# Performance work log

Hardware: AMD Instinct MI355X
Metric: run time of the kernel (lower is better)

## Reference

```python
import jax, jax.numpy as jnp
import numpy as np

B, D_IN, H, N_LAYERS, D_OUT = 262144, 8, 128, 3, 1


def setup_inputs() -> dict:
    key = jax.random.key(0)
    ks = jax.random.split(key, 18)
    rn = lambda k, shape, fan: (jax.random.normal(k, shape, jnp.float32) / np.sqrt(fan))
    return {
        "x": jax.random.normal(ks[0], (B, D_IN), jnp.float32),
        "Sw_w": rn(ks[1], (D_IN, H), D_IN),
        "Sw_b": rn(ks[2], (H,), D_IN),
        "Uz": rn(ks[3], (N_LAYERS, D_IN, H), D_IN),
        "Wsz_w": rn(ks[4], (N_LAYERS, H, H), H),
        "Wsz_b": rn(ks[5], (N_LAYERS, H), H),
        "Ug": rn(ks[6], (N_LAYERS, D_IN, H), D_IN),
        "Wsg_w": rn(ks[7], (N_LAYERS, H, H), H),
        "Wsg_b": rn(ks[8], (N_LAYERS, H), H),
        "Ur": rn(ks[9], (N_LAYERS, D_IN, H), D_IN),
        "Wsr_w": rn(ks[10], (N_LAYERS, H, H), H),
        "Wsr_b": rn(ks[11], (N_LAYERS, H), H),
        "Uh": rn(ks[12], (N_LAYERS, D_IN, H), D_IN),
        "Wsh_w": rn(ks[13], (N_LAYERS, H, H), H),
        "Wsh_b": rn(ks[14], (N_LAYERS, H), H),
        "Wf_w": rn(ks[15], (H, D_OUT), H),
        "Wf_b": rn(ks[16], (D_OUT,), H),
    }


def reference(x, Sw_w, Sw_b, Uz, Wsz_w, Wsz_b, Ug, Wsg_w, Wsg_b,
              Ur, Wsr_w, Wsr_b, Uh, Wsh_w, Wsh_b, Wf_w, Wf_b):
    # x: [B, D_in]; S: [B, H]
    S = x @ Sw_w + Sw_b
    n = Uz.shape[0]
    for i in range(n):  # small fixed layer count
        S = jax.nn.sigmoid(S)
        Z = jax.nn.sigmoid(x @ Uz[i] + S @ Wsz_w[i] + Wsz_b[i])
        G = jax.nn.sigmoid(x @ Ug[i] + S @ Wsg_w[i] + Wsg_b[i])
        R = jax.nn.sigmoid(x @ Ur[i] + S @ Wsr_w[i] + Wsr_b[i])
        H_ = jnp.tanh(x @ Uh[i] + (S * R) @ Wsh_w[i] + Wsh_b[i])
        S = (1.0 - G) * H_ + Z * S
    return S @ Wf_w + Wf_b  # [B, D_out]
```

## Files before the change

### kernel.cpp

```cpp
#include <hip/hip_runtime.h>

typedef __bf16 bf16_t;
typedef __bf16 bf16x4 __attribute__((ext_vector_type(4)));
typedef __bf16 bf16x8 __attribute__((ext_vector_type(8)));
typedef float f32x4 __attribute__((ext_vector_type(4)));

#define NL 3
#define HD 128
#define ROWS 64
#define SSTR 152
#define RSTR 136
#define THREADS 512
#define BATCH 262144
#define NBLK (BATCH / ROWS)

#define SW_OFF 0
#define U_OFF  4096
#define W_OFF  53248
#define WS_ELEMS 249856

#define MFMA(a, b, c) __builtin_amdgcn_mfma_f32_16x16x32_bf16((a), (b), (c), 0, 0, 0)

#define LOG2E 1.4426950408889634f
__device__ __forceinline__ float sige(float a) {
    return __builtin_amdgcn_rcpf(1.f + __builtin_amdgcn_exp2f(a));
}
__device__ __forceinline__ float tanhe(float a) {
    return 1.f - 2.f * __builtin_amdgcn_rcpf(__builtin_amdgcn_exp2f(a) + 1.f);
}
__device__ __forceinline__ float sigm(float v) {
    return __builtin_amdgcn_rcpf(1.f + __builtin_amdgcn_exp2f(-LOG2E * v));
}

__global__ void dgm_prep(const float* __restrict__ SwW, const float* __restrict__ Swb,
                         const float* __restrict__ Uz, const float* __restrict__ Wz, const float* __restrict__ Bz,
                         const float* __restrict__ Ug, const float* __restrict__ Wg, const float* __restrict__ Bg,
                         const float* __restrict__ Ur, const float* __restrict__ Wr, const float* __restrict__ Br,
                         const float* __restrict__ Uh, const float* __restrict__ Wh,
                         bf16_t* __restrict__ ws) {
    int idx = blockIdx.x * 256 + threadIdx.x;
    if (idx >= WS_ELEMS) return;
    const float* Us[4] = {Uz, Ug, Ur, Uh};
    const float* Wm[4] = {Wz, Wg, Wr, Wh};
    const float gsc[4] = {-LOG2E, LOG2E, -LOG2E, 2.f * LOG2E};
    if (idx < U_OFF) {
        int ct = idx >> 9, rem = idx & 511, lane = rem >> 3, j = rem & 7;
        int q = lane >> 4, mm = lane & 15;
        int k = q * 8 + j, n = ct * 16 + mm;
        float v = (k < 8) ? SwW[k * HD + n] : (k == 8) ? Swb[n] : 0.f;
        ws[idx] = (bf16_t)(v * -LOG2E);
    } else if (idx < W_OFF) {
        int t = idx - U_OFF;
        int lg = t >> 12, r2 = t & 4095;
        int l = lg >> 2, g = lg & 3;
        int ct = r2 >> 9, rem = r2 & 511, lane = rem >> 3, j = rem & 7;
        int q = lane >> 4, mm = lane & 15;
        int k = q * 8 + j, n = ct * 16 + mm;
        const float* Bs = (g == 0) ? Bz : (g == 1) ? Bg : (g == 2) ? Br : (const float*)0;
        float v = (k < 8) ? Us[g][(l * 8 + k) * HD + n]
                : (k == 8 && g < 3) ? Bs[l * HD + n] : 0.f;
        ws[idx] = (bf16_t)(v * gsc[g]);
    } else {
        int t = idx - W_OFF;
        int lg = t >> 14, r2 = t & 16383;
        int l = lg >> 2, g = lg & 3;
        int ct = r2 >> 11, kc = (r2 >> 9) & 3, rem = r2 & 511, lane = rem >> 3, j = rem & 7;
        int q = lane >> 4, mm = lane & 15;
        int k = kc * 32 + q * 8 + j, n = ct * 16 + mm;
        ws[idx] = (bf16_t)(Wm[g][(l * HD + k) * HD + n] * gsc[g]);
    }
}

__global__ __launch_bounds__(THREADS, 4) void dgm_main(
    const float* __restrict__ x,
    const float* __restrict__ Bh,
    const float* __restrict__ WfW, const float* __restrict__ WfB,
    const bf16_t* __restrict__ ws,
    float* __restrict__ out) {
    __shared__ __align__(16) bf16_t s_sig[2][ROWS * SSTR];
    __shared__ __align__(16) bf16_t s_r[ROWS * RSTR];
    __shared__ float red[ROWS];

    const int tid = threadIdx.x;
    const int lane = tid & 63;
    const int ct = tid >> 6;
    const int m = lane & 15, q = lane >> 4;
    const int rb = blockIdx.x * ROWS;
    const int f0 = ct * 16 + q * 4;
    const int fragoff = (ct * 64 + lane) * 8;
    const int wfragoff = (ct * 4) * 512 + lane * 8;
    const int xoff = 128 + (q ? 8 : 0);

    if (tid < ROWS) red[tid] = 0.f;

    {
        int r = tid >> 3, j = tid & 7;
        bf16_t xv = (bf16_t)x[(size_t)(rb + r) * 8 + j];
        s_sig[0][r * SSTR + 128 + j] = xv;
        s_sig[1][r * SSTR + 128 + j] = xv;
        s_r[r * RSTR + 128 + j] = xv;
        bf16_t ov = (j == 0) ? (bf16_t)1.f : (bf16_t)0.f;
        s_sig[0][r * SSTR + 136 + j] = ov;
        s_sig[1][r * SSTR + 136 + j] = ov;
    }
    __syncthreads();

    bf16x4 svp[4];

    {
        bf16x8 fSw = *(const bf16x8*)(ws + SW_OFF + fragoff);
#pragma unroll
        for (int bt = 0; bt < 4; bt++) {
            bf16x8 b = *(const bf16x8*)(&s_sig[0][(bt * 16 + m) * SSTR + xoff]);
            f32x4 acc = {0.f, 0.f, 0.f, 0.f};
            acc = MFMA(fSw, b, acc);
            bf16x4 pk;
#pragma unroll
            for (int i = 0; i < 4; i++) pk[i] = (bf16_t)sige(acc[i]);
            svp[bt] = pk;
            *(bf16x4*)(&s_sig[0][(bt * 16 + m) * SSTR + f0]) = pk;
        }
    }
    __syncthreads();

#pragma unroll 1
    for (int l = 0; l < NL; l++) {
        const int cur = l & 1, nxt = cur ^ 1;
        const bool last = (l == NL - 1);
        const bf16_t* wb = ws + W_OFF + (size_t)l * 4 * 16384;
        const bf16_t* ub = ws + U_OFF + (size_t)l * 4 * 4096;

        {
            bf16x8 fU = *(const bf16x8*)(ub + 2 * 4096 + fragoff);
            bf16x8 fW[4];
#pragma unroll
            for (int kc = 0; kc < 4; kc++)
                fW[kc] = *(const bf16x8*)(wb + 2 * 16384 + wfragoff + kc * 512);
#pragma unroll
            for (int bt = 0; bt < 4; bt++) {
                const bf16_t* bbase = &s_sig[cur][(bt * 16 + m) * SSTR];
                f32x4 aR = {0.f, 0.f, 0.f, 0.f};
#pragma unroll
                for (int kc = 0; kc < 4; kc++) {
                    bf16x8 b = *(const bf16x8*)(bbase + kc * 32 + q * 8);
                    aR = MFMA(fW[kc], b, aR);
                }
                {
                    bf16x8 b = *(const bf16x8*)(bbase + xoff);
                    aR = MFMA(fU, b, aR);
                }
                bf16x4 pk;
#pragma unroll
                for (int i = 0; i < 4; i++)
                    pk[i] = (bf16_t)(sige(aR[i]) * (float)svp[bt][i]);
                *(bf16x4*)(&s_r[(bt * 16 + m) * RSTR + f0]) = pk;
            }
        }
        __syncthreads();

        bf16x4 t1p[4];
        bf16x4 ogp[4];

        {
            bf16x8 fUz = *(const bf16x8*)(ub + 0 * 4096 + fragoff);
            bf16x8 fUg = *(const bf16x8*)(ub + 1 * 4096 + fragoff);
            bf16x8 fWz[4], fWg[4];
#pragma unroll
            for (int kc = 0; kc < 4; kc++) {
                fWz[kc] = *(const bf16x8*)(wb + 0 * 16384 + wfragoff + kc * 512);
                fWg[kc] = *(const bf16x8*)(wb + 1 * 16384 + wfragoff + kc * 512);
            }
#pragma unroll
            for (int bt = 0; bt < 4; bt++) {
                const bf16_t* bbase = &s_sig[cur][(bt * 16 + m) * SSTR];
                f32x4 aZ = {0.f, 0.f, 0.f, 0.f}, aG = {0.f, 0.f, 0.f, 0.f};
#pragma unroll
                for (int kc = 0; kc < 4; kc++) {
                    bf16x8 b = *(const bf16x8*)(bbase + kc * 32 + q * 8);
                    aZ = MFMA(fWz[kc], b, aZ);
                    aG = MFMA(fWg[kc], b, aG);
                }
                {
                    bf16x8 b = *(const bf16x8*)(bbase + xoff);
                    aZ = MFMA(fUz, b, aZ);
                    aG = MFMA(fUg, b, aG);
                }
                bf16x4 t1, og;
#pragma unroll
                for (int i = 0; i < 4; i++) {
                    t1[i] = (bf16_t)(sige(aZ[i]) * (float)svp[bt][i]);
                    og[i] = (bf16_t)sige(aG[i]);
                }
                t1p[bt] = t1;
                ogp[bt] = og;
            }
        }

        {
            bf16x8 fU = *(const bf16x8*)(ub + 3 * 4096 + fragoff);
            bf16x8 fW[4];
#pragma unroll
            for (int kc = 0; kc < 4; kc++)
                fW[kc] = *(const bf16x8*)(wb + 3 * 16384 + wfragoff + kc * 512);
            f32x4 bh4 = *(const f32x4*)&Bh[l * HD + f0];
#pragma unroll
            for (int i = 0; i < 4; i++) bh4[i] *= 2.f * LOG2E;
#pragma unroll
            for (int bt = 0; bt < 4; bt++) {
                const bf16_t* bbase = &s_r[(bt * 16 + m) * RSTR];
                f32x4 aH = {0.f, 0.f, 0.f, 0.f};
#pragma unroll
                for (int kc = 0; kc < 4; kc++) {
                    bf16x8 b = *(const bf16x8*)(bbase + kc * 32 + q * 8);
                    aH = MFMA(fW[kc], b, aH);
                }
                {
                    bf16x8 b = *(const bf16x8*)(bbase + 128);
                    aH = MFMA(fU, b, aH);
                }
                if (last) {
                    const f32x4 wf4 = *(const f32x4*)&WfW[f0];
                    float p = 0.f;
#pragma unroll
                    for (int i = 0; i < 4; i++) {
                        float hh = tanhe(aH[i] + bh4[i]);
                        float sn = (float)ogp[bt][i] * hh + (float)t1p[bt][i];
                        p += sn * wf4[i];
                    }
                    p += __shfl_xor(p, 16);
                    p += __shfl_xor(p, 32);
                    if (q == 0) atomicAdd(&red[bt * 16 + m], p);
                } else {
                    bf16x4 pk;
#pragma unroll
                    for (int i = 0; i < 4; i++) {
                        float hh = tanhe(aH[i] + bh4[i]);
                        float sn = (float)ogp[bt][i] * hh + (float)t1p[bt][i];
                        pk[i] = (bf16_t)sigm(sn);
                    }
                    svp[bt] = pk;
                    *(bf16x4*)(&s_sig[nxt][(bt * 16 + m) * SSTR + f0]) = pk;
                }
            }
        }
        __syncthreads();
    }

    if (tid < ROWS) out[rb + tid] = red[tid] + WfB[0];
}

extern "C" void kernel_launch(void* const* d_in, const int* in_sizes, int n_in,
                              void* d_out, int out_size, void* d_ws, size_t ws_size,
                              hipStream_t stream) {
    const float* x   = (const float*)d_in[0];
    const float* SwW = (const float*)d_in[1];
    const float* Swb = (const float*)d_in[2];
    const float* Uz  = (const float*)d_in[3];
    const float* Wz  = (const float*)d_in[4];
    const float* Bz  = (const float*)d_in[5];
    const float* Ug  = (const float*)d_in[6];
    const float* Wg  = (const float*)d_in[7];
    const float* Bg  = (const float*)d_in[8];
    const float* Ur  = (const float*)d_in[9];
    const float* Wr  = (const float*)d_in[10];
    const float* Br  = (const float*)d_in[11];
    const float* Uh  = (const float*)d_in[12];
    const float* Wh  = (const float*)d_in[13];
    const float* Bh  = (const float*)d_in[14];
    const float* WfW = (const float*)d_in[15];
    const float* WfB = (const float*)d_in[16];
    bf16_t* ws = (bf16_t*)d_ws;
    float* out = (float*)d_out;

    if (ws_size < (size_t)WS_ELEMS * sizeof(bf16_t)) return;

    dgm_prep<<<(WS_ELEMS + 255) / 256, 256, 0, stream>>>(SwW, Swb, Uz, Wz, Bz, Ug, Wg, Bg,
                                                         Ur, Wr, Br, Uh, Wh, ws);
    dgm_main<<<NBLK, THREADS, 0, stream>>>(x, Bh, WfW, WfB, ws, out);
}
```

Measured before the change: 264.6 us.

## Single-buffer state in LDS and split x tile to raise occupancy

```diff
diff --git a/kernel.cpp b/kernel.cpp
--- a/kernel.cpp
+++ b/kernel.cpp
@@ -8,8 +8,9 @@
 #define NL 3
 #define HD 128
 #define ROWS 64
-#define SSTR 152
+#define SSTR 136
 #define RSTR 136
+#define XSTR 24
 #define THREADS 512
 #define BATCH 262144
 #define NBLK (BATCH / ROWS)
@@ -71,14 +72,15 @@
     }
 }
 
-__global__ __launch_bounds__(THREADS, 4) void dgm_main(
+__global__ __launch_bounds__(THREADS, 8) void dgm_main(
     const float* __restrict__ x,
     const float* __restrict__ Bh,
     const float* __restrict__ WfW, const float* __restrict__ WfB,
     const bf16_t* __restrict__ ws,
     float* __restrict__ out) {
-    __shared__ __align__(16) bf16_t s_sig[2][ROWS * SSTR];
+    __shared__ __align__(16) bf16_t s_sig[ROWS * SSTR];
     __shared__ __align__(16) bf16_t s_r[ROWS * RSTR];
+    __shared__ __align__(16) bf16_t s_xo[ROWS * XSTR];
     __shared__ float red[ROWS];
 
     const int tid = threadIdx.x;
@@ -89,19 +91,14 @@
     const int f0 = ct * 16 + q * 4;
     const int fragoff = (ct * 64 + lane) * 8;
     const int wfragoff = (ct * 4) * 512 + lane * 8;
-    const int xoff = 128 + (q ? 8 : 0);
+    const int xoff = (q ? 8 : 0);
 
     if (tid < ROWS) red[tid] = 0.f;
 
     {
         int r = tid >> 3, j = tid & 7;
-        bf16_t xv = (bf16_t)x[(size_t)(rb + r) * 8 + j];
-        s_sig[0][r * SSTR + 128 + j] = xv;
-        s_sig[1][r * SSTR + 128 + j] = xv;
-        s_r[r * RSTR + 128 + j] = xv;
-        bf16_t ov = (j == 0) ? (bf16_t)1.f : (bf16_t)0.f;
-        s_sig[0][r * SSTR + 136 + j] = ov;
-        s_sig[1][r * SSTR + 136 + j] = ov;
+        s_xo[r * XSTR + j] = (bf16_t)x[(size_t)(rb + r) * 8 + j];
+        s_xo[r * XSTR + 8 + j] = (j == 0) ? (bf16_t)1.f : (bf16_t)0.f;
     }
     __syncthreads();
 
@@ -111,21 +108,20 @@
         bf16x8 fSw = *(const bf16x8*)(ws + SW_OFF + fragoff);
 #pragma unroll
         for (int bt = 0; bt < 4; bt++) {
-            bf16x8 b = *(const bf16x8*)(&s_sig[0][(bt * 16 + m) * SSTR + xoff]);
+            bf16x8 b = *(const bf16x8*)(&s_xo[(bt * 16 + m) * XSTR + xoff]);
             f32x4 acc = {0.f, 0.f, 0.f, 0.f};
             acc = MFMA(fSw, b, acc);
             bf16x4 pk;
 #pragma unroll
             for (int i = 0; i < 4; i++) pk[i] = (bf16_t)sige(acc[i]);
             svp[bt] = pk;
-            *(bf16x4*)(&s_sig[0][(bt * 16 + m) * SSTR + f0]) = pk;
+            *(bf16x4*)(&s_sig[(bt * 16 + m) * SSTR + f0]) = pk;
         }
     }
     __syncthreads();
 
 #pragma unroll 1
     for (int l = 0; l < NL; l++) {
-        const int cur = l & 1, nxt = cur ^ 1;
         const bool last = (l == NL - 1);
         const bf16_t* wb = ws + W_OFF + (size_t)l * 4 * 16384;
         const bf16_t* ub = ws + U_OFF + (size_t)l * 4 * 4096;
@@ -138,7 +134,8 @@
                 fW[kc] = *(const bf16x8*)(wb + 2 * 16384 + wfragoff + kc * 512);
 #pragma unroll
             for (int bt = 0; bt < 4; bt++) {
-                const bf16_t* bbase = &s_sig[cur][(bt * 16 + m) * SSTR];
+                const bf16_t* bbase = &s_sig[(bt * 16 + m) * SSTR];
+                const bf16_t* xbase = &s_xo[(bt * 16 + m) * XSTR];
                 f32x4 aR = {0.f, 0.f, 0.f, 0.f};
 #pragma unroll
                 for (int kc = 0; kc < 4; kc++) {
@@ -146,7 +143,7 @@
                     aR = MFMA(fW[kc], b, aR);
                 }
                 {
-                    bf16x8 b = *(const bf16x8*)(bbase + xoff);
+                    bf16x8 b = *(const bf16x8*)(xbase + xoff);
                     aR = MFMA(fU, b, aR);
                 }
                 bf16x4 pk;
@@ -172,7 +169,8 @@
             }
 #pragma unroll
             for (int bt = 0; bt < 4; bt++) {
-                const bf16_t* bbase = &s_sig[cur][(bt * 16 + m) * SSTR];
+                const bf16_t* bbase = &s_sig[(bt * 16 + m) * SSTR];
+                const bf16_t* xbase = &s_xo[(bt * 16 + m) * XSTR];
                 f32x4 aZ = {0.f, 0.f, 0.f, 0.f}, aG = {0.f, 0.f, 0.f, 0.f};
 #pragma unroll
                 for (int kc = 0; kc < 4; kc++) {
@@ -181,7 +179,7 @@
                     aG = MFMA(fWg[kc], b, aG);
                 }
                 {
-                    bf16x8 b = *(const bf16x8*)(bbase + xoff);
+                    bf16x8 b = *(const bf16x8*)(xbase + xoff);
                     aZ = MFMA(fUz, b, aZ);
                     aG = MFMA(fUg, b, aG);
                 }
@@ -195,6 +193,7 @@
                 ogp[bt] = og;
             }
         }
+        __syncthreads();
 
         {
             bf16x8 fU = *(const bf16x8*)(ub + 3 * 4096 + fragoff);
@@ -208,6 +207,7 @@
 #pragma unroll
             for (int bt = 0; bt < 4; bt++) {
                 const bf16_t* bbase = &s_r[(bt * 16 + m) * RSTR];
+                const bf16_t* xbase = &s_xo[(bt * 16 + m) * XSTR];
                 f32x4 aH = {0.f, 0.f, 0.f, 0.f};
 #pragma unroll
                 for (int kc = 0; kc < 4; kc++) {
@@ -215,7 +215,7 @@
                     aH = MFMA(fW[kc], b, aH);
                 }
                 {
-                    bf16x8 b = *(const bf16x8*)(bbase + 128);
+                    bf16x8 b = *(const bf16x8*)(xbase);
                     aH = MFMA(fU, b, aH);
                 }
                 if (last) {
@@ -239,7 +239,7 @@
                         pk[i] = (bf16_t)sigm(sn);
                     }
                     svp[bt] = pk;
-                    *(bf16x4*)(&s_sig[nxt][(bt * 16 + m) * SSTR + f0]) = pk;
+                    *(bf16x4*)(&s_sig[(bt * 16 + m) * SSTR + f0]) = pk;
                 }
             }
         }
```

Result: slower. 498.6 us (+88.5%).
